# Kernel optimization log

Hardware: AMD Instinct MI355X
Metric: run time of the kernel (lower is better)

The kernel has to match this reference:

```python
import jax, jax.numpy as jnp
import numpy as np

SIG = 10
C = 0.0
STD = 1.0
N_ATOMS = 21
N_TRAIN = 8192
DESC = N_ATOMS * (N_ATOMS - 1) // 2  # 210
M = 64


def setup_inputs() -> dict:
    key = jax.random.key(0)
    k1, k2, k3 = jax.random.split(key, 3)
    Rs = jax.random.normal(k1, (M, N_ATOMS, 3), dtype=jnp.float32)
    xs_train = jax.random.uniform(k2, (N_TRAIN, DESC), dtype=jnp.float32)
    Jx_alphas = jax.random.normal(k3, (N_TRAIN, DESC), dtype=jnp.float32)
    return {"Rs": Rs, "xs_train": xs_train, "Jx_alphas": Jx_alphas}


def reference(Rs, xs_train, Jx_alphas):
    sig = SIG
    q = np.sqrt(5.0) / sig
    n = N_ATOMS
    # pairwise atom displacements / distances: [M, n, n, 3], [M, n, n]
    diffs = Rs[:, :, None, :] - Rs[:, None, :, :]
    dists = jnp.linalg.norm(diffs, axis=-1)
    eye = jnp.eye(n, dtype=bool)
    dists = jnp.where(eye, jnp.inf, dists)  # kill diagonal
    i, j = np.tril_indices(n, k=-1)
    xs = 1.0 / dists[:, i, j]                       # [M, D] inverse-distance descriptor
    x_diffs = q * xs[:, None, :] - q * xs_train     # [M, T, D]
    x_dists = jnp.linalg.norm(x_diffs, axis=-1)     # [M, T]
    exp_xs = (5.0 / (3.0 * sig ** 2)) * jnp.exp(-x_dists)
    dot = jnp.einsum('mtd,td->mt', x_diffs, Jx_alphas)
    exp_xs_1 = exp_xs * (1.0 + x_dists)
    F1s_x = jnp.einsum('mt,mtd->md', exp_xs * dot, x_diffs)  # [M, D]
    F2s_x = exp_xs_1 @ Jx_alphas                              # [M, D]
    Fs_x = (F1s_x - F2s_x) * STD
    # expand_tril: scatter D lower-tri values to symmetric [M, n, n], zero diag
    full = jnp.zeros((Fs_x.shape[0], n, n), dtype=Fs_x.dtype)
    full = full.at[:, i, j].set(Fs_x).at[:, j, i].set(Fs_x)
    Fs = jnp.einsum('mab,mabc->mac', full / dists ** 3, diffs)  # diag: 0/inf -> 0
    Es = jnp.sum(exp_xs_1 * dot, axis=-1) / q
    Es = C + Es * STD
    return Es, Fs
```

## Files before the change

kernel.cpp:

```cpp
#include <hip/hip_runtime.h>
#include <math.h>

#define NA   21
#define NM   64
#define ND   210
#define DP   224
#define NT   8192
#define NCH  28

#define QC 0.22360679774997896f
#define KE 0.016666666666666666f

typedef short bf8 __attribute__((ext_vector_type(8)));
typedef float f4  __attribute__((ext_vector_type(4)));
typedef _Float16 h4 __attribute__((ext_vector_type(4)));

#define O_AF   0u
#define O_QG   7168u
#define O_NX   21504u
#define O_ESP  21568u
#define O_WAP  54336u
#define O_PB   87104u

__device__ __forceinline__ unsigned short f2bf(float f) {
    unsigned u = __float_as_uint(f);
    u += 0x7fffu + ((u >> 16) & 1u);
    return (unsigned short)(u >> 16);
}
__device__ __forceinline__ float bf2f(unsigned short h) {
    return __uint_as_float((unsigned)h << 16);
}

__device__ __forceinline__ void d_to_ij(int d, int& i, int& j) {
    int ii = (int)((1.0f + sqrtf(1.0f + 8.0f * (float)d)) * 0.5f);
    while (ii * (ii - 1) / 2 > d) --ii;
    while ((ii + 1) * ii / 2 <= d) ++ii;
    i = ii;
    j = d - ii * (ii - 1) / 2;
}

__global__ __launch_bounds__(256) void k_geom(
    const float* __restrict__ Rs, unsigned short* __restrict__ Af,
    float* __restrict__ qxsG, float* __restrict__ nx) {
    const int m = blockIdx.x, tid = threadIdx.x;
    __shared__ float R[NA * 3];
    __shared__ float red[256];
    if (tid < NA * 3) R[tid] = Rs[m * NA * 3 + tid];
    __syncthreads();
    float local = 0.0f;
    if (tid < DP) {
        float vr = 0.0f;
        unsigned short hv = 0;
        if (tid < ND) {
            int i, j; d_to_ij(tid, i, j);
            float dx = R[i * 3] - R[j * 3];
            float dy = R[i * 3 + 1] - R[j * 3 + 1];
            float dz = R[i * 3 + 2] - R[j * 3 + 2];
            float v = QC / sqrtf(dx * dx + dy * dy + dz * dz);
            hv = f2bf(v);
            vr = bf2f(hv);
        }
        Af[(((m >> 4) * NCH + (tid >> 3)) * 16 + (m & 15)) * 8 + (tid & 7)] = hv;
        qxsG[(tid >> 2) * 256 + m * 4 + (tid & 3)] = vr;
        local = vr * vr;
    }
    red[tid] = local;
    __syncthreads();
    for (int s = 128; s > 0; s >>= 1) {
        if (tid < s) red[tid] += red[tid + s];
        __syncthreads();
    }
    if (tid == 0) nx[m] = red[0];
}

__global__ __launch_bounds__(512) void k_s1p2(
    const float* __restrict__ xs, const float* __restrict__ Jx,
    const unsigned short* __restrict__ Af, const float* __restrict__ nxg,
    float* __restrict__ EsPart, float* __restrict__ WaPart,
    _Float16* __restrict__ Pbuf) {
    const int b = blockIdx.x, tid = threadIdx.x;
    const int lane = tid & 63;
    const int wave = tid >> 6;
    const int mtile = wave & 3, sub = wave >> 2;
    const int col = lane & 15, quad = lane >> 4;

    __shared__ unsigned short xJh[2 * 32 * DP];
    __shared__ unsigned short Dwh[64][33];
    __shared__ unsigned short Deh[64][33];
    __shared__ float ntL[32], cjL[32];
    char* xB = (char*)xJh;

    const unsigned short* ap = Af + ((size_t)(mtile * NCH + quad) * 16 + col) * 8;
    bf8 af[7];
#pragma unroll
    for (int kc = 0; kc < 7; ++kc) af[kc] = *(const bf8*)(ap + kc * 512);
    float nxv[4];
#pragma unroll
    for (int r = 0; r < 4; ++r) nxv[r] = nxg[mtile * 16 + quad * 4 + r];

    if (tid < 448) {
        const int arr = tid / 224, rem = tid - arr * 224;
        const int t = rem / 7, k2 = rem - t * 7;
        *(unsigned*)(xB + arr * 14336 +
                     (((unsigned)(t * 448 + 420 + k2 * 4)) ^ ((unsigned)((t & 7) << 4)))) = 0u;
    }
    const float2* sx = (const float2*)(xs + (size_t)b * 32 * ND);
    const float2* sj = (const float2*)(Jx + (size_t)b * 32 * ND);
#pragma unroll
    for (int k = 0; k < 7; ++k) {
        const int p = k * 512 + tid;
        if (p < 3360) {
            const float2 vx = sx[p];
            const float2 vj = sj[p];
            const int t = p / 105;
            const unsigned bo = ((unsigned)(4 * p + 28 * t)) ^ ((unsigned)((t & 7) << 4));
            *(unsigned*)(xB + bo) =
                (unsigned)f2bf(QC * vx.x) | ((unsigned)f2bf(QC * vx.y) << 16);
            *(unsigned*)(xB + 14336 + bo) =
                (unsigned)f2bf(vj.x) | ((unsigned)f2bf(vj.y) << 16);
        }
    }
    __syncthreads();

    const unsigned base0 = (unsigned)((sub * 16 + col) * 448 + quad * 16);
    const unsigned swc = (unsigned)((col & 7) << 4);
    bf8 bx[2], bj[2];
    bx[0] = *(const bf8*)(xB + (base0 ^ swc));
    bj[0] = *(const bf8*)(xB + 14336 + (base0 ^ swc));
    bx[1] = *(const bf8*)(xB + ((base0 + 64) ^ swc));
    bj[1] = *(const bf8*)(xB + 14336 + ((base0 + 64) ^ swc));
    f4 c1 = {0.f, 0.f, 0.f, 0.f};
    f4 c2 = {0.f, 0.f, 0.f, 0.f};
#pragma unroll
    for (int kc = 0; kc < 7; ++kc) {
        const int s = kc & 1;
        c1 = __builtin_amdgcn_mfma_f32_16x16x32_bf16(af[kc], bx[s], c1, 0, 0, 0);
        c2 = __builtin_amdgcn_mfma_f32_16x16x32_bf16(af[kc], bj[s], c2, 0, 0, 0);
        if (kc < 5) {
            bx[s] = *(const bf8*)(xB + ((base0 + (kc + 2) * 64) ^ swc));
            bj[s] = *(const bf8*)(xB + 14336 + ((base0 + (kc + 2) * 64) ^ swc));
        }
    }

    {
        const int tt = tid >> 4, l = tid & 15;
        const unsigned swt = (unsigned)((tt & 7) << 4);
        float sn = 0.0f, sc2 = 0.0f;
#pragma unroll
        for (int c = l; c < DP; c += 16) {
            const unsigned off = ((unsigned)(tt * 448 + 2 * c)) ^ swt;
            const float x = bf2f(*(const unsigned short*)(xB + off));
            const float jv = bf2f(*(const unsigned short*)(xB + 14336 + off));
            sn = fmaf(x, x, sn);
            sc2 = fmaf(x, jv, sc2);
        }
#pragma unroll
        for (int o = 1; o < 16; o <<= 1) {
            sn += __shfl_xor(sn, o);
            sc2 += __shfl_xor(sc2, o);
        }
        if (l == 0) { ntL[tt] = sn; cjL[tt] = sc2; }
    }
    __syncthreads();

    const int tloc = sub * 16 + col;
    const float ntv = ntL[tloc], cjv = cjL[tloc];
    float esA[4], wlA[4];
#pragma unroll
    for (int r = 0; r < 4; ++r) {
        const int m = mtile * 16 + quad * 4 + r;
        float sq = fmaxf(nxv[r] - 2.0f * c1[r] + ntv, 0.0f);
        float xd = sqrtf(sq);
        float e = KE * expf(-xd);
        float dotv = c2[r] - cjv;
        float wv = e * dotv;
        float ev = e * (1.0f + xd);
        Dwh[m][tloc] = f2bf(wv);
        Deh[m][tloc] = f2bf(ev);
        esA[r] = ev * dotv;
        wlA[r] = wv;
    }
#pragma unroll
    for (int r = 0; r < 4; ++r) {
        float e = esA[r], wl = wlA[r];
#pragma unroll
        for (int o = 1; o < 16; o <<= 1) {
            e += __shfl_xor(e, o);
            wl += __shfl_xor(wl, o);
        }
        if (col == 0) {
            const int m = mtile * 16 + quad * 4 + r;
            EsPart[(size_t)m * 512 + b * 2 + sub] = e;
            WaPart[(size_t)m * 512 + b * 2 + sub] = wl;
        }
    }
    __syncthreads();

    union { unsigned short us[8]; bf8 v; } uaw, uae;
#pragma unroll
    for (int i = 0; i < 8; ++i) {
        uaw.us[i] = Dwh[mtile * 16 + col][quad * 8 + i];
        uae.us[i] = Deh[mtile * 16 + col][quad * 8 + i];
    }
    const int dt0 = sub * 7;
#pragma unroll
    for (int dd = 0; dd < 7; ++dd) {
        const int dt = dt0 + dd;
        union { unsigned short us[8]; bf8 v; } ubx, ubj;
#pragma unroll
        for (int i = 0; i < 8; ++i) {
            const int t = quad * 8 + i;
            const unsigned off =
                ((unsigned)(t * 448 + 2 * (dt * 16 + col))) ^ ((unsigned)((t & 7) << 4));
            ubx.us[i] = *(const unsigned short*)(xB + off);
            ubj.us[i] = *(const unsigned short*)(xB + 14336 + off);
        }
        f4 z = {0.f, 0.f, 0.f, 0.f};
        f4 dA = __builtin_amdgcn_mfma_f32_16x16x32_bf16(uaw.v, ubx.v, z, 0, 0, 0);
        f4 dB = __builtin_amdgcn_mfma_f32_16x16x32_bf16(uae.v, ubj.v, z, 0, 0, 0);
#pragma unroll
        for (int r = 0; r < 4; ++r) {
            const int m = mtile * 16 + quad * 4 + r;
            Pbuf[((size_t)(m * 256 + b)) * DP + dt * 16 + col] =
                (_Float16)(dA[r] + dB[r]);
        }
    }
}

__global__ __launch_bounds__(1024) void k_final(
    const float* __restrict__ Rs, const float* __restrict__ qxsG,
    const _Float16* __restrict__ Pbuf, const float* __restrict__ EsPart,
    const float* __restrict__ WaPart, float* __restrict__ out) {
    int m = blockIdx.x, tid = threadIdx.x;
    __shared__ float R[NA * 3];
    __shared__ float Ff[NA][NA];
    __shared__ float redE[256];
    __shared__ float redW[256];
    __shared__ float ABp[16][DP];
    if (tid < NA * 3) R[tid] = Rs[m * NA * 3 + tid];
    if (tid < NA) Ff[tid][tid] = 0.0f;
    {
        const int g = tid >> 6, l = tid & 63;
        const int d0 = l * 4;
        if (d0 < DP) {
            const _Float16* p0 = Pbuf + (size_t)m * 256 * DP + (size_t)g * 16 * DP + d0;
            float s0 = 0.0f, s1 = 0.0f, s2 = 0.0f, s3 = 0.0f;
#pragma unroll
            for (int bb = 0; bb < 16; ++bb) {
                const h4 v = *(const h4*)(p0 + bb * DP);
                s0 += (float)v[0];
                s1 += (float)v[1];
                s2 += (float)v[2];
                s3 += (float)v[3];
            }
            ABp[g][d0] = s0;
            ABp[g][d0 + 1] = s1;
            ABp[g][d0 + 2] = s2;
            ABp[g][d0 + 3] = s3;
        }
    }
    if (tid < 256) {
        const float2 ep = ((const float2*)(EsPart + (size_t)m * 512))[tid];
        const float2 wp = ((const float2*)(WaPart + (size_t)m * 512))[tid];
        redE[tid] = ep.x + ep.y;
        redW[tid] = wp.x + wp.y;
    }
    __syncthreads();
    for (int s = 128; s > 0; s >>= 1) {
        if (tid < s) {
            redE[tid] += redE[tid + s];
            redW[tid] += redW[tid + s];
        }
        __syncthreads();
    }
    const float Wa = redW[0];
    if (tid < ND) {
        int i, j; d_to_ij(tid, i, j);
        float dx = R[i * 3] - R[j * 3];
        float dy = R[i * 3 + 1] - R[j * 3 + 1];
        float dz = R[i * 3 + 2] - R[j * 3 + 2];
        float dist2 = dx * dx + dy * dy + dz * dz;
        float ab = 0.0f;
#pragma unroll
        for (int g = 0; g < 16; ++g) ab += ABp[g][tid];
        float fsx = qxsG[(tid >> 2) * 256 + m * 4 + (tid & 3)] * Wa - ab;
        float f = fsx / (dist2 * sqrtf(dist2));
        Ff[i][j] = f;
        Ff[j][i] = f;
    }
    __syncthreads();
    if (tid < NA * 3) {
        int a = tid / 3, c = tid % 3;
        float s = 0.0f;
        for (int b = 0; b < NA; ++b) {
            if (b == a) continue;
            s += Ff[a][b] * (R[a * 3 + c] - R[b * 3 + c]);
        }
        out[NM + m * NA * 3 + tid] = s;
    }
    if (tid == 0) out[m] = redE[0] / QC;
}

extern "C" void kernel_launch(void* const* d_in, const int* in_sizes, int n_in,
                              void* d_out, int out_size, void* d_ws, size_t ws_size,
                              hipStream_t stream) {
    const float* Rs = (const float*)d_in[0];
    const float* xs_train = (const float*)d_in[1];
    const float* Jx_alphas = (const float*)d_in[2];
    float* out = (float*)d_out;
    float* ws = (float*)d_ws;

    unsigned short* Af = (unsigned short*)(ws + O_AF);
    float* qxsG   = ws + O_QG;
    float* nx     = ws + O_NX;
    float* EsPart = ws + O_ESP;
    float* WaPart = ws + O_WAP;
    _Float16* Pbuf = (_Float16*)(ws + O_PB);

    k_geom<<<NM, 256, 0, stream>>>(Rs, Af, qxsG, nx);
    k_s1p2<<<256, 512, 0, stream>>>(xs_train, Jx_alphas, Af, nx,
                                    EsPart, WaPart, Pbuf);
    k_final<<<NM, 1024, 0, stream>>>(Rs, qxsG, Pbuf, EsPart, WaPart, out);
}
```

Before: 84.94 us.

## Fuse three kernels into one cooperative kernel with grid-wide syncs

Merges the geometry, main MFMA stage, and final reduction kernels into a single cooperative launch of 256 blocks of 512 threads, separated by grid.sync barriers. The goal is to remove two kernel launch gaps. The final stage now runs with 512 threads per block, so each thread reduces 32 partial rows instead of 16. This adds the cost of grid-wide barriers and of cooperative launch, and the final stage has less parallelism than before.

```diff
diff --git a/kernel.cpp b/kernel.cpp
--- a/kernel.cpp
+++ b/kernel.cpp
@@ -1,5 +1,8 @@
 #include <hip/hip_runtime.h>
+#include <hip/hip_cooperative_groups.h>
 #include <math.h>
+
+namespace cg = cooperative_groups;
 
 #define NA   21
 #define NM   64
@@ -39,266 +42,268 @@
     j = d - ii * (ii - 1) / 2;
 }
 
-__global__ __launch_bounds__(256) void k_geom(
-    const float* __restrict__ Rs, unsigned short* __restrict__ Af,
-    float* __restrict__ qxsG, float* __restrict__ nx) {
-    const int m = blockIdx.x, tid = threadIdx.x;
-    __shared__ float R[NA * 3];
-    __shared__ float red[256];
-    if (tid < NA * 3) R[tid] = Rs[m * NA * 3 + tid];
-    __syncthreads();
-    float local = 0.0f;
-    if (tid < DP) {
-        float vr = 0.0f;
-        unsigned short hv = 0;
-        if (tid < ND) {
-            int i, j; d_to_ij(tid, i, j);
-            float dx = R[i * 3] - R[j * 3];
-            float dy = R[i * 3 + 1] - R[j * 3 + 1];
-            float dz = R[i * 3 + 2] - R[j * 3 + 2];
-            float v = QC / sqrtf(dx * dx + dy * dy + dz * dz);
-            hv = f2bf(v);
-            vr = bf2f(hv);
-        }
-        Af[(((m >> 4) * NCH + (tid >> 3)) * 16 + (m & 15)) * 8 + (tid & 7)] = hv;
-        qxsG[(tid >> 2) * 256 + m * 4 + (tid & 3)] = vr;
-        local = vr * vr;
-    }
-    red[tid] = local;
-    __syncthreads();
-    for (int s = 128; s > 0; s >>= 1) {
-        if (tid < s) red[tid] += red[tid + s];
-        __syncthreads();
-    }
-    if (tid == 0) nx[m] = red[0];
-}
-
-__global__ __launch_bounds__(512) void k_s1p2(
+__global__ __launch_bounds__(512) void k_all(
     const float* __restrict__ xs, const float* __restrict__ Jx,
-    const unsigned short* __restrict__ Af, const float* __restrict__ nxg,
+    const float* __restrict__ Rs,
+    unsigned short* __restrict__ Af, float* __restrict__ qxsG,
+    float* __restrict__ nxg,
     float* __restrict__ EsPart, float* __restrict__ WaPart,
-    _Float16* __restrict__ Pbuf) {
+    _Float16* __restrict__ Pbuf, float* __restrict__ out) {
     const int b = blockIdx.x, tid = threadIdx.x;
     const int lane = tid & 63;
     const int wave = tid >> 6;
     const int mtile = wave & 3, sub = wave >> 2;
     const int col = lane & 15, quad = lane >> 4;
 
-    __shared__ unsigned short xJh[2 * 32 * DP];
+    __shared__ __align__(16) unsigned short xJh[2 * 32 * DP];
     __shared__ unsigned short Dwh[64][33];
     __shared__ unsigned short Deh[64][33];
     __shared__ float ntL[32], cjL[32];
     char* xB = (char*)xJh;
 
-    const unsigned short* ap = Af + ((size_t)(mtile * NCH + quad) * 16 + col) * 8;
-    bf8 af[7];
-#pragma unroll
-    for (int kc = 0; kc < 7; ++kc) af[kc] = *(const bf8*)(ap + kc * 512);
-    float nxv[4];
-#pragma unroll
-    for (int r = 0; r < 4; ++r) nxv[r] = nxg[mtile * 16 + quad * 4 + r];
-
-    if (tid < 448) {
-        const int arr = tid / 224, rem = tid - arr * 224;
-        const int t = rem / 7, k2 = rem - t * 7;
-        *(unsigned*)(xB + arr * 14336 +
-                     (((unsigned)(t * 448 + 420 + k2 * 4)) ^ ((unsigned)((t & 7) << 4)))) = 0u;
+    if (b < NM) {
+        float* Rg  = (float*)xB;
+        float* red = (float*)(xB + 256);
+        if (tid < NA * 3) Rg[tid] = Rs[b * NA * 3 + tid];
+        __syncthreads();
+        float local = 0.0f;
+        if (tid < DP) {
+            float vr = 0.0f;
+            unsigned short hv = 0;
+            if (tid < ND) {
+                int i, j; d_to_ij(tid, i, j);
+                float dx = Rg[i * 3] - Rg[j * 3];
+                float dy = Rg[i * 3 + 1] - Rg[j * 3 + 1];
+                float dz = Rg[i * 3 + 2] - Rg[j * 3 + 2];
+                float v = QC / sqrtf(dx * dx + dy * dy + dz * dz);
+                hv = f2bf(v);
+                vr = bf2f(hv);
+            }
+            Af[(((b >> 4) * NCH + (tid >> 3)) * 16 + (b & 15)) * 8 + (tid & 7)] = hv;
+            qxsG[(tid >> 2) * 256 + b * 4 + (tid & 3)] = vr;
+            local = vr * vr;
+        }
+        if (tid < 256) red[tid] = local;
+        __syncthreads();
+        for (int s = 128; s > 0; s >>= 1) {
+            if (tid < s) red[tid] += red[tid + s];
+            __syncthreads();
+        }
+        if (tid == 0) nxg[b] = red[0];
     }
-    const float2* sx = (const float2*)(xs + (size_t)b * 32 * ND);
-    const float2* sj = (const float2*)(Jx + (size_t)b * 32 * ND);
-#pragma unroll
-    for (int k = 0; k < 7; ++k) {
-        const int p = k * 512 + tid;
-        if (p < 3360) {
-            const float2 vx = sx[p];
-            const float2 vj = sj[p];
-            const int t = p / 105;
-            const unsigned bo = ((unsigned)(4 * p + 28 * t)) ^ ((unsigned)((t & 7) << 4));
-            *(unsigned*)(xB + bo) =
-                (unsigned)f2bf(QC * vx.x) | ((unsigned)f2bf(QC * vx.y) << 16);
-            *(unsigned*)(xB + 14336 + bo) =
-                (unsigned)f2bf(vj.x) | ((unsigned)f2bf(vj.y) << 16);
-        }
-    }
-    __syncthreads();
-
-    const unsigned base0 = (unsigned)((sub * 16 + col) * 448 + quad * 16);
-    const unsigned swc = (unsigned)((col & 7) << 4);
-    bf8 bx[2], bj[2];
-    bx[0] = *(const bf8*)(xB + (base0 ^ swc));
-    bj[0] = *(const bf8*)(xB + 14336 + (base0 ^ swc));
-    bx[1] = *(const bf8*)(xB + ((base0 + 64) ^ swc));
-    bj[1] = *(const bf8*)(xB + 14336 + ((base0 + 64) ^ swc));
-    f4 c1 = {0.f, 0.f, 0.f, 0.f};
-    f4 c2 = {0.f, 0.f, 0.f, 0.f};
-#pragma unroll
-    for (int kc = 0; kc < 7; ++kc) {
-        const int s = kc & 1;
-        c1 = __builtin_amdgcn_mfma_f32_16x16x32_bf16(af[kc], bx[s], c1, 0, 0, 0);
-        c2 = __builtin_amdgcn_mfma_f32_16x16x32_bf16(af[kc], bj[s], c2, 0, 0, 0);
-        if (kc < 5) {
-            bx[s] = *(const bf8*)(xB + ((base0 + (kc + 2) * 64) ^ swc));
-            bj[s] = *(const bf8*)(xB + 14336 + ((base0 + (kc + 2) * 64) ^ swc));
-        }
-    }
+    __threadfence();
+    cg::this_grid().sync();
 
     {
-        const int tt = tid >> 4, l = tid & 15;
-        const unsigned swt = (unsigned)((tt & 7) << 4);
-        float sn = 0.0f, sc2 = 0.0f;
-#pragma unroll
-        for (int c = l; c < DP; c += 16) {
-            const unsigned off = ((unsigned)(tt * 448 + 2 * c)) ^ swt;
-            const float x = bf2f(*(const unsigned short*)(xB + off));
-            const float jv = bf2f(*(const unsigned short*)(xB + 14336 + off));
-            sn = fmaf(x, x, sn);
-            sc2 = fmaf(x, jv, sc2);
-        }
-#pragma unroll
-        for (int o = 1; o < 16; o <<= 1) {
-            sn += __shfl_xor(sn, o);
-            sc2 += __shfl_xor(sc2, o);
-        }
-        if (l == 0) { ntL[tt] = sn; cjL[tt] = sc2; }
-    }
-    __syncthreads();
-
-    const int tloc = sub * 16 + col;
-    const float ntv = ntL[tloc], cjv = cjL[tloc];
-    float esA[4], wlA[4];
-#pragma unroll
-    for (int r = 0; r < 4; ++r) {
-        const int m = mtile * 16 + quad * 4 + r;
-        float sq = fmaxf(nxv[r] - 2.0f * c1[r] + ntv, 0.0f);
-        float xd = sqrtf(sq);
-        float e = KE * expf(-xd);
-        float dotv = c2[r] - cjv;
-        float wv = e * dotv;
-        float ev = e * (1.0f + xd);
-        Dwh[m][tloc] = f2bf(wv);
-        Deh[m][tloc] = f2bf(ev);
-        esA[r] = ev * dotv;
-        wlA[r] = wv;
-    }
-#pragma unroll
-    for (int r = 0; r < 4; ++r) {
-        float e = esA[r], wl = wlA[r];
-#pragma unroll
-        for (int o = 1; o < 16; o <<= 1) {
-            e += __shfl_xor(e, o);
-            wl += __shfl_xor(wl, o);
-        }
-        if (col == 0) {
-            const int m = mtile * 16 + quad * 4 + r;
-            EsPart[(size_t)m * 512 + b * 2 + sub] = e;
-            WaPart[(size_t)m * 512 + b * 2 + sub] = wl;
-        }
-    }
-    __syncthreads();
-
-    union { unsigned short us[8]; bf8 v; } uaw, uae;
-#pragma unroll
-    for (int i = 0; i < 8; ++i) {
-        uaw.us[i] = Dwh[mtile * 16 + col][quad * 8 + i];
-        uae.us[i] = Deh[mtile * 16 + col][quad * 8 + i];
-    }
-    const int dt0 = sub * 7;
-#pragma unroll
-    for (int dd = 0; dd < 7; ++dd) {
-        const int dt = dt0 + dd;
-        union { unsigned short us[8]; bf8 v; } ubx, ubj;
-#pragma unroll
-        for (int i = 0; i < 8; ++i) {
-            const int t = quad * 8 + i;
-            const unsigned off =
-                ((unsigned)(t * 448 + 2 * (dt * 16 + col))) ^ ((unsigned)((t & 7) << 4));
-            ubx.us[i] = *(const unsigned short*)(xB + off);
-            ubj.us[i] = *(const unsigned short*)(xB + 14336 + off);
-        }
-        f4 z = {0.f, 0.f, 0.f, 0.f};
-        f4 dA = __builtin_amdgcn_mfma_f32_16x16x32_bf16(uaw.v, ubx.v, z, 0, 0, 0);
-        f4 dB = __builtin_amdgcn_mfma_f32_16x16x32_bf16(uae.v, ubj.v, z, 0, 0, 0);
+        const unsigned short* ap = Af + ((size_t)(mtile * NCH + quad) * 16 + col) * 8;
+        bf8 af[7];
+#pragma unroll
+        for (int kc = 0; kc < 7; ++kc) af[kc] = *(const bf8*)(ap + kc * 512);
+        float nxv[4];
+#pragma unroll
+        for (int r = 0; r < 4; ++r) nxv[r] = nxg[mtile * 16 + quad * 4 + r];
+
+        if (tid < 448) {
+            const int arr = tid / 224, rem = tid - arr * 224;
+            const int t = rem / 7, k2 = rem - t * 7;
+            *(unsigned*)(xB + arr * 14336 +
+                         (((unsigned)(t * 448 + 420 + k2 * 4)) ^ ((unsigned)((t & 7) << 4)))) = 0u;
+        }
+        const float2* sx = (const float2*)(xs + (size_t)b * 32 * ND);
+        const float2* sj = (const float2*)(Jx + (size_t)b * 32 * ND);
+#pragma unroll
+        for (int k = 0; k < 7; ++k) {
+            const int p = k * 512 + tid;
+            if (p < 3360) {
+                const float2 vx = sx[p];
+                const float2 vj = sj[p];
+                const int t = p / 105;
+                const unsigned bo = ((unsigned)(4 * p + 28 * t)) ^ ((unsigned)((t & 7) << 4));
+                *(unsigned*)(xB + bo) =
+                    (unsigned)f2bf(QC * vx.x) | ((unsigned)f2bf(QC * vx.y) << 16);
+                *(unsigned*)(xB + 14336 + bo) =
+                    (unsigned)f2bf(vj.x) | ((unsigned)f2bf(vj.y) << 16);
+            }
+        }
+        __syncthreads();
+
+        const unsigned base0 = (unsigned)((sub * 16 + col) * 448 + quad * 16);
+        const unsigned swc = (unsigned)((col & 7) << 4);
+        bf8 bx[2], bj[2];
+        bx[0] = *(const bf8*)(xB + (base0 ^ swc));
+        bj[0] = *(const bf8*)(xB + 14336 + (base0 ^ swc));
+        bx[1] = *(const bf8*)(xB + ((base0 + 64) ^ swc));
+        bj[1] = *(const bf8*)(xB + 14336 + ((base0 + 64) ^ swc));
+        f4 c1 = {0.f, 0.f, 0.f, 0.f};
+        f4 c2 = {0.f, 0.f, 0.f, 0.f};
+#pragma unroll
+        for (int kc = 0; kc < 7; ++kc) {
+            const int s = kc & 1;
+            c1 = __builtin_amdgcn_mfma_f32_16x16x32_bf16(af[kc], bx[s], c1, 0, 0, 0);
+            c2 = __builtin_amdgcn_mfma_f32_16x16x32_bf16(af[kc], bj[s], c2, 0, 0, 0);
+            if (kc < 5) {
+                bx[s] = *(const bf8*)(xB + ((base0 + (kc + 2) * 64) ^ swc));
+                bj[s] = *(const bf8*)(xB + 14336 + ((base0 + (kc + 2) * 64) ^ swc));
+            }
+        }
+
+        {
+            const int tt = tid >> 4, l = tid & 15;
+            const unsigned swt = (unsigned)((tt & 7) << 4);
+            float sn = 0.0f, sc2 = 0.0f;
+#pragma unroll
+            for (int c = l; c < DP; c += 16) {
+                const unsigned off = ((unsigned)(tt * 448 + 2 * c)) ^ swt;
+                const float x = bf2f(*(const unsigned short*)(xB + off));
+                const float jv = bf2f(*(const unsigned short*)(xB + 14336 + off));
+                sn = fmaf(x, x, sn);
+                sc2 = fmaf(x, jv, sc2);
+            }
+#pragma unroll
+            for (int o = 1; o < 16; o <<= 1) {
+                sn += __shfl_xor(sn, o);
+                sc2 += __shfl_xor(sc2, o);
+            }
+            if (l == 0) { ntL[tt] = sn; cjL[tt] = sc2; }
+        }
+        __syncthreads();
+
+        const int tloc = sub * 16 + col;
+        const float ntv = ntL[tloc], cjv = cjL[tloc];
+        float esA[4], wlA[4];
 #pragma unroll
         for (int r = 0; r < 4; ++r) {
             const int m = mtile * 16 + quad * 4 + r;
-            Pbuf[((size_t)(m * 256 + b)) * DP + dt * 16 + col] =
-                (_Float16)(dA[r] + dB[r]);
+            float sq = fmaxf(nxv[r] - 2.0f * c1[r] + ntv, 0.0f);
+            float xd = sqrtf(sq);
+            float e = KE * expf(-xd);
+            float dotv = c2[r] - cjv;
+            float wv = e * dotv;
+            float ev = e * (1.0f + xd);
+            Dwh[m][tloc] = f2bf(wv);
+            Deh[m][tloc] = f2bf(ev);
+            esA[r] = ev * dotv;
+            wlA[r] = wv;
+        }
+#pragma unroll
+        for (int r = 0; r < 4; ++r) {
+            float e = esA[r], wl = wlA[r];
+#pragma unroll
+            for (int o = 1; o < 16; o <<= 1) {
+                e += __shfl_xor(e, o);
+                wl += __shfl_xor(wl, o);
+            }
+            if (col == 0) {
+                const int m = mtile * 16 + quad * 4 + r;
+                EsPart[(size_t)m * 512 + b * 2 + sub] = e;
+                WaPart[(size_t)m * 512 + b * 2 + sub] = wl;
+            }
+        }
+        __syncthreads();
+
+        union { unsigned short us[8]; bf8 v; } uaw, uae;
+#pragma unroll
+        for (int i = 0; i < 8; ++i) {
+            uaw.us[i] = Dwh[mtile * 16 + col][quad * 8 + i];
+            uae.us[i] = Deh[mtile * 16 + col][quad * 8 + i];
+        }
+        const int dt0 = sub * 7;
+#pragma unroll
+        for (int dd = 0; dd < 7; ++dd) {
+            const int dt = dt0 + dd;
+            union { unsigned short us[8]; bf8 v; } ubx, ubj;
+#pragma unroll
+            for (int i = 0; i < 8; ++i) {
+                const int t = quad * 8 + i;
+                const unsigned off =
+                    ((unsigned)(t * 448 + 2 * (dt * 16 + col))) ^ ((unsigned)((t & 7) << 4));
+                ubx.us[i] = *(const unsigned short*)(xB + off);
+                ubj.us[i] = *(const unsigned short*)(xB + 14336 + off);
+            }
+            f4 z = {0.f, 0.f, 0.f, 0.f};
+            f4 dA = __builtin_amdgcn_mfma_f32_16x16x32_bf16(uaw.v, ubx.v, z, 0, 0, 0);
+            f4 dB = __builtin_amdgcn_mfma_f32_16x16x32_bf16(uae.v, ubj.v, z, 0, 0, 0);
+#pragma unroll
+            for (int r = 0; r < 4; ++r) {
+                const int m = mtile * 16 + quad * 4 + r;
+                Pbuf[((size_t)(m * 256 + b)) * DP + dt * 16 + col] =
+                    (_Float16)(dA[r] + dB[r]);
+            }
         }
     }
-}
-
-__global__ __launch_bounds__(1024) void k_final(
-    const float* __restrict__ Rs, const float* __restrict__ qxsG,
-    const _Float16* __restrict__ Pbuf, const float* __restrict__ EsPart,
-    const float* __restrict__ WaPart, float* __restrict__ out) {
-    int m = blockIdx.x, tid = threadIdx.x;
-    __shared__ float R[NA * 3];
-    __shared__ float Ff[NA][NA];
-    __shared__ float redE[256];
-    __shared__ float redW[256];
-    __shared__ float ABp[16][DP];
-    if (tid < NA * 3) R[tid] = Rs[m * NA * 3 + tid];
-    if (tid < NA) Ff[tid][tid] = 0.0f;
-    {
-        const int g = tid >> 6, l = tid & 63;
-        const int d0 = l * 4;
-        if (d0 < DP) {
-            const _Float16* p0 = Pbuf + (size_t)m * 256 * DP + (size_t)g * 16 * DP + d0;
-            float s0 = 0.0f, s1 = 0.0f, s2 = 0.0f, s3 = 0.0f;
-#pragma unroll
-            for (int bb = 0; bb < 16; ++bb) {
-                const h4 v = *(const h4*)(p0 + bb * DP);
-                s0 += (float)v[0];
-                s1 += (float)v[1];
-                s2 += (float)v[2];
-                s3 += (float)v[3];
-            }
-            ABp[g][d0] = s0;
-            ABp[g][d0 + 1] = s1;
-            ABp[g][d0 + 2] = s2;
-            ABp[g][d0 + 3] = s3;
-        }
+    __threadfence();
+    cg::this_grid().sync();
+
+    if (b < NM) {
+        const int m = b;
+        float* Rf   = (float*)xB;
+        float (*Ff)[NA] = (float(*)[NA])(xB + 256);
+        float* redE = (float*)(xB + 2048);
+        float* redW = (float*)(xB + 3072);
+        float (*ABp)[DP] = (float(*)[DP])(xB + 4096);
+        if (tid < NA * 3) Rf[tid] = Rs[m * NA * 3 + tid];
+        if (tid < NA) Ff[tid][tid] = 0.0f;
+        {
+            const int g = tid >> 6, l = tid & 63;
+            const int d0 = l * 4;
+            if (d0 < DP) {
+                const _Float16* p0 = Pbuf + (size_t)m * 256 * DP + (size_t)g * 32 * DP + d0;
+                float s0 = 0.0f, s1 = 0.0f, s2 = 0.0f, s3 = 0.0f;
+#pragma unroll
+                for (int bb = 0; bb < 32; ++bb) {
+                    const h4 v = *(const h4*)(p0 + bb * DP);
+                    s0 += (float)v[0];
+                    s1 += (float)v[1];
+                    s2 += (float)v[2];
+                    s3 += (float)v[3];
+                }
+                ABp[g][d0] = s0;
+                ABp[g][d0 + 1] = s1;
+                ABp[g][d0 + 2] = s2;
+                ABp[g][d0 + 3] = s3;
+            }
+        }
+        if (tid < 256) {
+            const float2 ep = ((const float2*)(EsPart + (size_t)m * 512))[tid];
+            const float2 wp = ((const float2*)(WaPart + (size_t)m * 512))[tid];
+            redE[tid] = ep.x + ep.y;
+            redW[tid] = wp.x + wp.y;
+        }
+        __syncthreads();
+        for (int s = 128; s > 0; s >>= 1) {
+            if (tid < s) {
+                redE[tid] += redE[tid + s];
+                redW[tid] += redW[tid + s];
+            }
+            __syncthreads();
+        }
+        const float Wa = redW[0];
+        if (tid < ND) {
+            int i, j; d_to_ij(tid, i, j);
+            float dx = Rf[i * 3] - Rf[j * 3];
+            float dy = Rf[i * 3 + 1] - Rf[j * 3 + 1];
+            float dz = Rf[i * 3 + 2] - Rf[j * 3 + 2];
+            float dist2 = dx * dx + dy * dy + dz * dz;
+            float ab = 0.0f;
+#pragma unroll
+            for (int g = 0; g < 8; ++g) ab += ABp[g][tid];
+            float fsx = qxsG[(tid >> 2) * 256 + m * 4 + (tid & 3)] * Wa - ab;
+            float f = fsx / (dist2 * sqrtf(dist2));
+            Ff[i][j] = f;
+            Ff[j][i] = f;
+        }
+        __syncthreads();
+        if (tid < NA * 3) {
+            int a = tid / 3, c = tid % 3;
+            float s = 0.0f;
+            for (int bb2 = 0; bb2 < NA; ++bb2) {
+                if (bb2 == a) continue;
+                s += Ff[a][bb2] * (Rf[a * 3 + c] - Rf[bb2 * 3 + c]);
+            }
+            out[NM + m * NA * 3 + tid] = s;
+        }
+        if (tid == 0) out[m] = redE[0] / QC;
     }
-    if (tid < 256) {
-        const float2 ep = ((const float2*)(EsPart + (size_t)m * 512))[tid];
-        const float2 wp = ((const float2*)(WaPart + (size_t)m * 512))[tid];
-        redE[tid] = ep.x + ep.y;
-        redW[tid] = wp.x + wp.y;
-    }
-    __syncthreads();
-    for (int s = 128; s > 0; s >>= 1) {
-        if (tid < s) {
-            redE[tid] += redE[tid + s];
-            redW[tid] += redW[tid + s];
-        }
-        __syncthreads();
-    }
-    const float Wa = redW[0];
-    if (tid < ND) {
-        int i, j; d_to_ij(tid, i, j);
-        float dx = R[i * 3] - R[j * 3];
-        float dy = R[i * 3 + 1] - R[j * 3 + 1];
-        float dz = R[i * 3 + 2] - R[j * 3 + 2];
-        float dist2 = dx * dx + dy * dy + dz * dz;
-        float ab = 0.0f;
-#pragma unroll
-        for (int g = 0; g < 16; ++g) ab += ABp[g][tid];
-        float fsx = qxsG[(tid >> 2) * 256 + m * 4 + (tid & 3)] * Wa - ab;
-        float f = fsx / (dist2 * sqrtf(dist2));
-        Ff[i][j] = f;
-        Ff[j][i] = f;
-    }
-    __syncthreads();
-    if (tid < NA * 3) {
-        int a = tid / 3, c = tid % 3;
-        float s = 0.0f;
-        for (int b = 0; b < NA; ++b) {
-            if (b == a) continue;
-            s += Ff[a][b] * (R[a * 3 + c] - R[b * 3 + c]);
-        }
-        out[NM + m * NA * 3 + tid] = s;
-    }
-    if (tid == 0) out[m] = redE[0] / QC;
 }
 
 extern "C" void kernel_launch(void* const* d_in, const int* in_sizes, int n_in,
@@ -317,8 +322,9 @@
     float* WaPart = ws + O_WAP;
     _Float16* Pbuf = (_Float16*)(ws + O_PB);
 
-    k_geom<<<NM, 256, 0, stream>>>(Rs, Af, qxsG, nx);
-    k_s1p2<<<256, 512, 0, stream>>>(xs_train, Jx_alphas, Af, nx,
-                                    EsPart, WaPart, Pbuf);
-    k_final<<<NM, 1024, 0, stream>>>(Rs, qxsG, Pbuf, EsPart, WaPart, out);
-}
+    void* args[] = {(void*)&xs_train, (void*)&Jx_alphas, (void*)&Rs,
+                    (void*)&Af, (void*)&qxsG, (void*)&nx,
+                    (void*)&EsPart, (void*)&WaPart, (void*)&Pbuf, (void*)&out};
+    hipLaunchCooperativeKernel((const void*)k_all, dim3(256), dim3(512),
+                               args, 0, stream);
+}
```

Result: slower. 252.6 us (+197.4%).
